# Performance work log

Hardware: AMD Instinct MI355X
Metric: run time of the kernel (lower is better)

Reference implementation:

```python
import jax, jax.numpy as jnp
import numpy as np

B, H_C, W_C = 4, 256, 256        # coarse mask logits
C, H_F, W_F = 128, 512, 512      # fine feature map
N_POINTS = 8192
HIDDEN = 256


def _grid_sample_bilinear(img, grid):
    """Bilinear grid_sample, align_corners=False, zeros padding.
    img: [C,H,W]; grid: [N,2] with (x,y) in [-1,1]. Returns [N,C]."""
    Ci, H, W = img.shape
    x = ((grid[:, 0] + 1.0) * W - 1.0) * 0.5
    y = ((grid[:, 1] + 1.0) * H - 1.0) * 0.5
    x0 = jnp.floor(x); y0 = jnp.floor(y)
    x1 = x0 + 1.0; y1 = y0 + 1.0
    wx1 = x - x0; wx0 = 1.0 - wx1
    wy1 = y - y0; wy0 = 1.0 - wy1

    def gather(xi, yi):
        valid = (xi >= 0) & (xi < W) & (yi >= 0) & (yi < H)
        xc = jnp.clip(xi, 0, W - 1).astype(jnp.int32)
        yc = jnp.clip(yi, 0, H - 1).astype(jnp.int32)
        v = img[:, yc, xc]                       # [C,N]
        return v * valid.astype(img.dtype)

    out = (gather(x0, y0) * (wx0 * wy0)
           + gather(x1, y0) * (wx1 * wy0)
           + gather(x0, y1) * (wx0 * wy1)
           + gather(x1, y1) * (wx1 * wy1))       # [C,N]
    return out.T                                  # [N,C]


def setup_inputs() -> dict:
    key = jax.random.key(0)
    k1, k2, k3, k4 = jax.random.split(key, 4)
    coarse_logits = jax.random.normal(k1, (B, 1, H_C, W_C), dtype=jnp.float32)
    fine_feat = jax.random.normal(k2, (B, C, H_F, W_F), dtype=jnp.float32)
    W1 = jax.random.normal(k3, (C + 1, HIDDEN), dtype=jnp.float32) * (1.0 / np.sqrt(C + 1))
    b1 = jnp.zeros((HIDDEN,), dtype=jnp.float32)
    W2 = jax.random.normal(k4, (HIDDEN, 1), dtype=jnp.float32) * (1.0 / np.sqrt(HIDDEN))
    b2 = jnp.zeros((1,), dtype=jnp.float32)
    return {"coarse_logits": coarse_logits, "fine_feat": fine_feat,
            "W1": W1, "b1": b1, "W2": W2, "b2": b2, "num_points": N_POINTS}


def reference(coarse_logits, fine_feat, W1, b1, W2, b2, num_points):
    b, _, h, w = coarse_logits.shape
    # uncertainty = -|logits|  (calculate_uncertainty)
    unc = -jnp.abs(coarse_logits[:, 0])                       # [B,h,w]
    _, idx = jax.lax.top_k(unc.reshape(b, -1), num_points)    # [B,N]
    # pixel-center normalized coords (sampling_points eval branch): (x,y) in [0,1]
    h_step, w_step = 1.0 / h, 1.0 / w
    px = w_step / 2.0 + (idx % w).astype(jnp.float32) * w_step
    py = h_step / 2.0 + (idx // w).astype(jnp.float32) * h_step
    grid = 2.0 * jnp.stack([px, py], axis=-1) - 1.0           # [B,N,2] in [-1,1]
    # point_sample: bilinear gather of fine features at sampled points
    fine_pts = jax.vmap(_grid_sample_bilinear)(fine_feat, grid)   # [B,N,C]
    # point_sample_by_idx: gather coarse logits at flat indices
    coarse_flat = coarse_logits.reshape(b, -1)                 # [B,h*w]
    coarse_pts = jnp.take_along_axis(coarse_flat, idx, axis=1)[..., None]  # [B,N,1]
    # point head MLP on concat(fine, coarse)
    feats = jnp.concatenate([fine_pts, coarse_pts], axis=-1)   # [B,N,C+1]
    hid = jax.nn.relu(jnp.einsum('bnf,fk->bnk', feats, W1) + b1)
    refined = jnp.einsum('bnk,ko->bno', hid, W2) + b2          # [B,N,1]
    # scatter refined logits back into the coarse map at sampled indices
    out_flat = coarse_flat.at[jnp.arange(b)[:, None], idx].set(refined[..., 0])
    return out_flat.reshape(b, 1, h, w)
```

## Files before the change

kernel.cpp:

```cpp
#include <hip/hip_runtime.h>
#include <stdint.h>

#define B_ 4
#define HC 256
#define WC 256
#define C_ 128
#define HF 512
#define WF 512
#define NPTS 8192
#define HIDDEN_ 256
#define NPIX (HC*WC)
#define PPB 16
#define FSTRIDE 132

__global__ void pr_copy_kernel(const float4* __restrict__ src, float4* __restrict__ dst, int n4) {
    int i = blockIdx.x * blockDim.x + threadIdx.x;
    if (i < n4) dst[i] = src[i];
}

__global__ __launch_bounds__(1024) void pr_select_kernel(const float* __restrict__ coarse,
                                                         int* __restrict__ sel) {
    int b = blockIdx.x;
    const float* cb = coarse + (size_t)b * NPIX;
    int tid = threadIdx.x;
    int lane = tid & 63, wid = tid >> 6;

    __shared__ unsigned hist[256];
    __shared__ unsigned s_prefix;
    __shared__ int s_remk;
    __shared__ unsigned wsum[16];
    __shared__ unsigned s_chosen, s_cless;
    __shared__ unsigned warp_eq[16], warp_take[16];
    __shared__ unsigned s_eqbase, s_outbase;

    if (tid == 0) { s_prefix = 0u; s_remk = NPTS; }

    for (int pass = 0; pass < 4; ++pass) {
        if (tid < 256) hist[tid] = 0u;
        __syncthreads();
        unsigned prefix = s_prefix;
        int remk = s_remk;
        int shift = 24 - 8 * pass;

        if (pass == 0) {
            for (int i = 4 * tid; i < NPIX; i += 4096) {
                float4 v = *(const float4*)(cb + i);
                unsigned bins[4];
                bins[0] = (__float_as_uint(v.x) & 0x7fffffffu) >> 24;
                bins[1] = (__float_as_uint(v.y) & 0x7fffffffu) >> 24;
                bins[2] = (__float_as_uint(v.z) & 0x7fffffffu) >> 24;
                bins[3] = (__float_as_uint(v.w) & 0x7fffffffu) >> 24;
#pragma unroll
                for (int e = 0; e < 4; ++e) {
                    unsigned bin = bins[e];
                    unsigned long long am = ~0ull;
                    while (am) {
                        int leader = __ffsll((unsigned long long)am) - 1;
                        unsigned lbin = __shfl(bin, leader, 64);
                        unsigned long long match = __ballot(bin == lbin);
                        if (lane == leader) atomicAdd(&hist[lbin], (unsigned)__popcll(match));
                        am &= ~match;
                    }
                }
            }
        } else {
            for (int i = 4 * tid; i < NPIX; i += 4096) {
                float4 v = *(const float4*)(cb + i);
                unsigned k0 = __float_as_uint(v.x) & 0x7fffffffu;
                unsigned k1 = __float_as_uint(v.y) & 0x7fffffffu;
                unsigned k2 = __float_as_uint(v.z) & 0x7fffffffu;
                unsigned k3 = __float_as_uint(v.w) & 0x7fffffffu;
                if ((k0 >> (shift + 8)) == prefix) atomicAdd(&hist[(k0 >> shift) & 0xffu], 1u);
                if ((k1 >> (shift + 8)) == prefix) atomicAdd(&hist[(k1 >> shift) & 0xffu], 1u);
                if ((k2 >> (shift + 8)) == prefix) atomicAdd(&hist[(k2 >> shift) & 0xffu], 1u);
                if ((k3 >> (shift + 8)) == prefix) atomicAdd(&hist[(k3 >> shift) & 0xffu], 1u);
            }
        }
        __syncthreads();

        unsigned h = 0, incl = 0;
        if (tid < 256) {
            h = hist[tid];
            incl = h;
#pragma unroll
            for (int d = 1; d < 64; d <<= 1) {
                unsigned y = __shfl_up(incl, d, 64);
                if (lane >= d) incl += y;
            }
            if (lane == 63) wsum[wid] = incl;
        }
        __syncthreads();
        if (tid < 256) {
            unsigned base = 0;
            for (int w = 0; w < wid; ++w) base += wsum[w];
            unsigned inc = base + incl;
            unsigned exc = inc - h;
            if ((unsigned)remk > exc && (unsigned)remk <= inc) { s_chosen = (unsigned)tid; s_cless = exc; }
        }
        __syncthreads();
        if (tid == 0) { s_prefix = (s_prefix << 8) | s_chosen; s_remk = remk - (int)s_cless; }
        __syncthreads();
    }

    unsigned T = s_prefix;
    unsigned need_eq = (unsigned)s_remk;
    if (tid == 0) { s_eqbase = 0u; s_outbase = 0u; }
    __syncthreads();

    unsigned long long ltmask = (1ull << lane) - 1ull;
    for (int base = 0; base < NPIX; base += 4096) {
        int i0 = base + 4 * tid;
        float4 v = *(const float4*)(cb + i0);
        unsigned k[4];
        k[0] = __float_as_uint(v.x) & 0x7fffffffu;
        k[1] = __float_as_uint(v.y) & 0x7fffffffu;
        k[2] = __float_as_uint(v.z) & 0x7fffffffu;
        k[3] = __float_as_uint(v.w) & 0x7fffffffu;
        bool lt[4], eq[4];
        unsigned long long me[4];
        unsigned weq = 0;
#pragma unroll
        for (int e = 0; e < 4; ++e) {
            lt[e] = k[e] < T;
            eq[e] = k[e] == T;
            me[e] = __ballot(eq[e]);
            weq += (unsigned)__popcll(me[e]);
        }
        if (lane == 0) warp_eq[wid] = weq;
        __syncthreads();

        unsigned eqwb = 0, eqtot = 0;
        for (int w = 0; w < 16; ++w) { unsigned hh = warp_eq[w]; if (w < wid) eqwb += hh; eqtot += hh; }
        unsigned lt_lanes_eq = 0;
#pragma unroll
        for (int e = 0; e < 4; ++e) lt_lanes_eq += (unsigned)__popcll(me[e] & ltmask);
        unsigned ebase = s_eqbase + eqwb + lt_lanes_eq;

        bool take[4];
        unsigned long long mt[4];
        unsigned self_eq = 0;
#pragma unroll
        for (int e = 0; e < 4; ++e) {
            unsigned eqrank = ebase + self_eq;
            take[e] = lt[e] || (eq[e] && eqrank < need_eq);
            self_eq += eq[e] ? 1u : 0u;
        }
        unsigned wtk = 0;
#pragma unroll
        for (int e = 0; e < 4; ++e) {
            mt[e] = __ballot(take[e]);
            wtk += (unsigned)__popcll(mt[e]);
        }
        if (lane == 0) warp_take[wid] = wtk;
        __syncthreads();

        unsigned twb = 0, ttot = 0;
        for (int w = 0; w < 16; ++w) { unsigned hh = warp_take[w]; if (w < wid) twb += hh; ttot += hh; }
        unsigned lt_lanes_tk = 0;
#pragma unroll
        for (int e = 0; e < 4; ++e) lt_lanes_tk += (unsigned)__popcll(mt[e] & ltmask);
        unsigned tbase = s_outbase + twb + lt_lanes_tk;
        unsigned self_tk = 0;
#pragma unroll
        for (int e = 0; e < 4; ++e) {
            if (take[e]) sel[b * NPTS + (int)(tbase + self_tk)] = i0 + e;
            self_tk += take[e] ? 1u : 0u;
        }
        __syncthreads();
        if (tid == 0) { s_eqbase += eqtot; s_outbase += ttot; }
    }
}

__global__ __launch_bounds__(256) void pr_mlp_kernel(
    const float* __restrict__ coarse, const float* __restrict__ fine,
    const float* __restrict__ W1, const float* __restrict__ b1,
    const float* __restrict__ W2, const float* __restrict__ b2,
    const int* __restrict__ sel, float* __restrict__ out) {

    __shared__ __align__(16) float feats[PPB * FSTRIDE];
    __shared__ int sidx[PPB];
    __shared__ float red[PPB][4];

    int tid = threadIdx.x;
    const int bpb = NPTS / PPB;
    int b = blockIdx.x / bpb;
    int pbase = (blockIdx.x % bpb) * PPB;

    if (tid < PPB) sidx[tid] = sel[b * NPTS + pbase + tid];
    __syncthreads();

    const float* fb = fine + (size_t)b * (C_ * HF * WF);
    int c = tid & 127;
    int ph = tid >> 7;

    float2 r0[PPB / 2], r1[PPB / 2];
#pragma unroll
    for (int k = 0; k < PPB / 2; ++k) {
        int p = 2 * k + ph;
        int id = sidx[p];
        int ix = id & (WC - 1), iy = id >> 8;
        const float* a = fb + (size_t)c * (HF * WF) + (size_t)(2 * iy) * WF + 2 * ix;
        r0[k] = *(const float2*)a;
        r1[k] = *(const float2*)(a + WF);
    }
#pragma unroll
    for (int k = 0; k < PPB / 2; ++k) {
        int p = 2 * k + ph;
        feats[p * FSTRIDE + c] = 0.25f * ((r0[k].x + r0[k].y) + (r1[k].x + r1[k].y));
    }
    if (tid < PPB) feats[tid * FSTRIDE + 128] = coarse[(size_t)b * NPIX + sidx[tid]];
    __syncthreads();

    int j = tid;
    float acc[PPB];
    float b1j = b1[j];
#pragma unroll
    for (int p = 0; p < PPB; ++p) acc[p] = b1j;

    const float4* fs4 = (const float4*)feats;
#pragma unroll 4
    for (int f4 = 0; f4 < 32; ++f4) {
        float w0 = W1[(4 * f4 + 0) * HIDDEN_ + j];
        float w1 = W1[(4 * f4 + 1) * HIDDEN_ + j];
        float w2 = W1[(4 * f4 + 2) * HIDDEN_ + j];
        float w3 = W1[(4 * f4 + 3) * HIDDEN_ + j];
#pragma unroll
        for (int p = 0; p < PPB; ++p) {
            float4 fv = fs4[p * (FSTRIDE / 4) + f4];
            acc[p] = fmaf(fv.x, w0, acc[p]);
            acc[p] = fmaf(fv.y, w1, acc[p]);
            acc[p] = fmaf(fv.z, w2, acc[p]);
            acc[p] = fmaf(fv.w, w3, acc[p]);
        }
    }
    {
        float w128 = W1[128 * HIDDEN_ + j];
#pragma unroll
        for (int p = 0; p < PPB; ++p) acc[p] = fmaf(feats[p * FSTRIDE + 128], w128, acc[p]);
    }

    float w2j = W2[j];
    int lane = tid & 63, wid = tid >> 6;
#pragma unroll
    for (int p = 0; p < PPB; ++p) {
        float v = fmaxf(acc[p], 0.0f) * w2j;
        v += __shfl_down(v, 32, 64);
        v += __shfl_down(v, 16, 64);
        v += __shfl_down(v, 8, 64);
        v += __shfl_down(v, 4, 64);
        v += __shfl_down(v, 2, 64);
        v += __shfl_down(v, 1, 64);
        if (lane == 0) red[p][wid] = v;
    }
    __syncthreads();
    if (tid < PPB) {
        float r = red[tid][0] + red[tid][1] + red[tid][2] + red[tid][3] + b2[0];
        out[(size_t)b * NPIX + sidx[tid]] = r;
    }
}

extern "C" void kernel_launch(void* const* d_in, const int* in_sizes, int n_in,
                              void* d_out, int out_size, void* d_ws, size_t ws_size,
                              hipStream_t stream) {
    const float* coarse = (const float*)d_in[0];
    const float* fine   = (const float*)d_in[1];
    const float* W1     = (const float*)d_in[2];
    const float* b1     = (const float*)d_in[3];
    const float* W2     = (const float*)d_in[4];
    const float* b2     = (const float*)d_in[5];
    float* out = (float*)d_out;
    int* sel = (int*)d_ws;

    int n4 = B_ * NPIX / 4;
    pr_copy_kernel<<<(n4 + 255) / 256, 256, 0, stream>>>((const float4*)coarse, (float4*)out, n4);
    pr_select_kernel<<<B_, 1024, 0, stream>>>(coarse, sel);
    pr_mlp_kernel<<<B_ * (NPTS / PPB), 256, 0, stream>>>(coarse, fine, W1, b1, W2, b2, sel, out);
}
```

Measured before the change: 797.0 us.

## Split gather from MLP, privatize select histograms, retile MLP per wave

The select kernel now keeps eight privatized shared-memory histograms (one per pair of waves) to reduce atomic contention, summing them before the prefix scan. The fused gather+MLP kernel is split in two. A gather kernel with 2 points per block writes 2x2-averaged fine features plus the coarse logit to a global workspace. An MLP kernel then has each wave handle 8 points with each lane owning 4 hidden units, using float4 W1 loads and no cross-wave reduction. This is meant to expose more parallelism for the scattered fine-feature loads and raise arithmetic intensity in the MLP. The cost is an extra global round trip for features and one more kernel launch.

```diff
diff --git a/kernel.cpp b/kernel.cpp
--- a/kernel.cpp
+++ b/kernel.cpp
@@ -10,8 +10,7 @@
 #define NPTS 8192
 #define HIDDEN_ 256
 #define NPIX (HC*WC)
-#define PPB 16
-#define FSTRIDE 132
+#define GSTRIDE 132
 
 __global__ void pr_copy_kernel(const float4* __restrict__ src, float4* __restrict__ dst, int n4) {
     int i = blockIdx.x * blockDim.x + threadIdx.x;
@@ -24,8 +23,9 @@
     const float* cb = coarse + (size_t)b * NPIX;
     int tid = threadIdx.x;
     int lane = tid & 63, wid = tid >> 6;
-
-    __shared__ unsigned hist[256];
+    int hc = wid >> 1;
+
+    __shared__ unsigned hist[8][256];
     __shared__ unsigned s_prefix;
     __shared__ int s_remk;
     __shared__ unsigned wsum[16];
@@ -36,7 +36,7 @@
     if (tid == 0) { s_prefix = 0u; s_remk = NPTS; }
 
     for (int pass = 0; pass < 4; ++pass) {
-        if (tid < 256) hist[tid] = 0u;
+        for (int i = tid; i < 2048; i += 1024) ((unsigned*)hist)[i] = 0u;
         __syncthreads();
         unsigned prefix = s_prefix;
         int remk = s_remk;
@@ -58,7 +58,7 @@
                         int leader = __ffsll((unsigned long long)am) - 1;
                         unsigned lbin = __shfl(bin, leader, 64);
                         unsigned long long match = __ballot(bin == lbin);
-                        if (lane == leader) atomicAdd(&hist[lbin], (unsigned)__popcll(match));
+                        if (lane == leader) atomicAdd(&hist[hc][lbin], (unsigned)__popcll(match));
                         am &= ~match;
                     }
                 }
@@ -70,17 +70,18 @@
                 unsigned k1 = __float_as_uint(v.y) & 0x7fffffffu;
                 unsigned k2 = __float_as_uint(v.z) & 0x7fffffffu;
                 unsigned k3 = __float_as_uint(v.w) & 0x7fffffffu;
-                if ((k0 >> (shift + 8)) == prefix) atomicAdd(&hist[(k0 >> shift) & 0xffu], 1u);
-                if ((k1 >> (shift + 8)) == prefix) atomicAdd(&hist[(k1 >> shift) & 0xffu], 1u);
-                if ((k2 >> (shift + 8)) == prefix) atomicAdd(&hist[(k2 >> shift) & 0xffu], 1u);
-                if ((k3 >> (shift + 8)) == prefix) atomicAdd(&hist[(k3 >> shift) & 0xffu], 1u);
+                if ((k0 >> (shift + 8)) == prefix) atomicAdd(&hist[hc][(k0 >> shift) & 0xffu], 1u);
+                if ((k1 >> (shift + 8)) == prefix) atomicAdd(&hist[hc][(k1 >> shift) & 0xffu], 1u);
+                if ((k2 >> (shift + 8)) == prefix) atomicAdd(&hist[hc][(k2 >> shift) & 0xffu], 1u);
+                if ((k3 >> (shift + 8)) == prefix) atomicAdd(&hist[hc][(k3 >> shift) & 0xffu], 1u);
             }
         }
         __syncthreads();
 
         unsigned h = 0, incl = 0;
         if (tid < 256) {
-            h = hist[tid];
+            h = hist[0][tid] + hist[1][tid] + hist[2][tid] + hist[3][tid]
+              + hist[4][tid] + hist[5][tid] + hist[6][tid] + hist[7][tid];
             incl = h;
 #pragma unroll
             for (int d = 1; d < 64; d <<= 1) {
@@ -171,91 +172,105 @@
     }
 }
 
+__global__ __launch_bounds__(256) void pr_gather_kernel(
+    const float* __restrict__ coarse, const float* __restrict__ fine,
+    const int* __restrict__ sel, float* __restrict__ feats) {
+    int tid = threadIdx.x;
+    int b = blockIdx.x >> 12;
+    int pbase = (blockIdx.x & 4095) * 2;
+    __shared__ int sidx[2];
+    if (tid < 2) sidx[tid] = sel[b * NPTS + pbase + tid];
+    __syncthreads();
+    int c = tid & 127, ph = tid >> 7;
+    int id = sidx[ph];
+    int ix = id & (WC - 1), iy = id >> 8;
+    const float* a = fine + (size_t)(b * C_ + c) * (HF * WF) + (size_t)(2 * iy) * WF + 2 * ix;
+    float2 r0 = *(const float2*)a;
+    float2 r1 = *(const float2*)(a + WF);
+    size_t o = (size_t)(b * NPTS + pbase + ph) * GSTRIDE;
+    feats[o + c] = 0.25f * ((r0.x + r0.y) + (r1.x + r1.y));
+    if (c == 0) feats[o + 128] = coarse[(size_t)b * NPIX + id];
+}
+
 __global__ __launch_bounds__(256) void pr_mlp_kernel(
-    const float* __restrict__ coarse, const float* __restrict__ fine,
-    const float* __restrict__ W1, const float* __restrict__ b1,
-    const float* __restrict__ W2, const float* __restrict__ b2,
-    const int* __restrict__ sel, float* __restrict__ out) {
-
-    __shared__ __align__(16) float feats[PPB * FSTRIDE];
-    __shared__ int sidx[PPB];
-    __shared__ float red[PPB][4];
-
+    const float* __restrict__ feats, const float* __restrict__ W1,
+    const float* __restrict__ b1, const float* __restrict__ W2,
+    const float* __restrict__ b2, const int* __restrict__ sel,
+    float* __restrict__ out) {
+    __shared__ int sidx[32];
     int tid = threadIdx.x;
-    const int bpb = NPTS / PPB;
-    int b = blockIdx.x / bpb;
-    int pbase = (blockIdx.x % bpb) * PPB;
-
-    if (tid < PPB) sidx[tid] = sel[b * NPTS + pbase + tid];
+    int b = blockIdx.x >> 8;
+    int pbase = (blockIdx.x & 255) * 32;
+    if (tid < 32) sidx[tid] = sel[b * NPTS + pbase + tid];
     __syncthreads();
 
-    const float* fb = fine + (size_t)b * (C_ * HF * WF);
-    int c = tid & 127;
-    int ph = tid >> 7;
-
-    float2 r0[PPB / 2], r1[PPB / 2];
-#pragma unroll
-    for (int k = 0; k < PPB / 2; ++k) {
-        int p = 2 * k + ph;
-        int id = sidx[p];
-        int ix = id & (WC - 1), iy = id >> 8;
-        const float* a = fb + (size_t)c * (HF * WF) + (size_t)(2 * iy) * WF + 2 * ix;
-        r0[k] = *(const float2*)a;
-        r1[k] = *(const float2*)(a + WF);
-    }
-#pragma unroll
-    for (int k = 0; k < PPB / 2; ++k) {
-        int p = 2 * k + ph;
-        feats[p * FSTRIDE + c] = 0.25f * ((r0[k].x + r0[k].y) + (r1[k].x + r1[k].y));
-    }
-    if (tid < PPB) feats[tid * FSTRIDE + 128] = coarse[(size_t)b * NPIX + sidx[tid]];
-    __syncthreads();
-
-    int j = tid;
-    float acc[PPB];
-    float b1j = b1[j];
-#pragma unroll
-    for (int p = 0; p < PPB; ++p) acc[p] = b1j;
-
-    const float4* fs4 = (const float4*)feats;
-#pragma unroll 4
+    int lane = tid & 63, wv = tid >> 6;
+    float4 b14 = *(const float4*)&b1[4 * lane];
+    float acc[8][4];
+#pragma unroll
+    for (int i = 0; i < 8; ++i) {
+        acc[i][0] = b14.x; acc[i][1] = b14.y; acc[i][2] = b14.z; acc[i][3] = b14.w;
+    }
+
+    const float* frow = feats + (size_t)(b * NPTS + pbase + wv * 8) * GSTRIDE;
+    const float4* f4p = (const float4*)frow;
+
     for (int f4 = 0; f4 < 32; ++f4) {
-        float w0 = W1[(4 * f4 + 0) * HIDDEN_ + j];
-        float w1 = W1[(4 * f4 + 1) * HIDDEN_ + j];
-        float w2 = W1[(4 * f4 + 2) * HIDDEN_ + j];
-        float w3 = W1[(4 * f4 + 3) * HIDDEN_ + j];
-#pragma unroll
-        for (int p = 0; p < PPB; ++p) {
-            float4 fv = fs4[p * (FSTRIDE / 4) + f4];
-            acc[p] = fmaf(fv.x, w0, acc[p]);
-            acc[p] = fmaf(fv.y, w1, acc[p]);
-            acc[p] = fmaf(fv.z, w2, acc[p]);
-            acc[p] = fmaf(fv.w, w3, acc[p]);
+        float4 w0 = *(const float4*)&W1[(4 * f4 + 0) * HIDDEN_ + 4 * lane];
+        float4 w1v = *(const float4*)&W1[(4 * f4 + 1) * HIDDEN_ + 4 * lane];
+        float4 w2v = *(const float4*)&W1[(4 * f4 + 2) * HIDDEN_ + 4 * lane];
+        float4 w3v = *(const float4*)&W1[(4 * f4 + 3) * HIDDEN_ + 4 * lane];
+#pragma unroll
+        for (int i = 0; i < 8; ++i) {
+            float4 fv = f4p[i * 33 + f4];
+            acc[i][0] = fmaf(fv.x, w0.x, acc[i][0]);
+            acc[i][1] = fmaf(fv.x, w0.y, acc[i][1]);
+            acc[i][2] = fmaf(fv.x, w0.z, acc[i][2]);
+            acc[i][3] = fmaf(fv.x, w0.w, acc[i][3]);
+            acc[i][0] = fmaf(fv.y, w1v.x, acc[i][0]);
+            acc[i][1] = fmaf(fv.y, w1v.y, acc[i][1]);
+            acc[i][2] = fmaf(fv.y, w1v.z, acc[i][2]);
+            acc[i][3] = fmaf(fv.y, w1v.w, acc[i][3]);
+            acc[i][0] = fmaf(fv.z, w2v.x, acc[i][0]);
+            acc[i][1] = fmaf(fv.z, w2v.y, acc[i][1]);
+            acc[i][2] = fmaf(fv.z, w2v.z, acc[i][2]);
+            acc[i][3] = fmaf(fv.z, w2v.w, acc[i][3]);
+            acc[i][0] = fmaf(fv.w, w3v.x, acc[i][0]);
+            acc[i][1] = fmaf(fv.w, w3v.y, acc[i][1]);
+            acc[i][2] = fmaf(fv.w, w3v.z, acc[i][2]);
+            acc[i][3] = fmaf(fv.w, w3v.w, acc[i][3]);
         }
     }
     {
-        float w128 = W1[128 * HIDDEN_ + j];
-#pragma unroll
-        for (int p = 0; p < PPB; ++p) acc[p] = fmaf(feats[p * FSTRIDE + 128], w128, acc[p]);
-    }
-
-    float w2j = W2[j];
-    int lane = tid & 63, wid = tid >> 6;
-#pragma unroll
-    for (int p = 0; p < PPB; ++p) {
-        float v = fmaxf(acc[p], 0.0f) * w2j;
+        float4 wl = *(const float4*)&W1[128 * HIDDEN_ + 4 * lane];
+#pragma unroll
+        for (int i = 0; i < 8; ++i) {
+            float fc = frow[i * GSTRIDE + 128];
+            acc[i][0] = fmaf(fc, wl.x, acc[i][0]);
+            acc[i][1] = fmaf(fc, wl.y, acc[i][1]);
+            acc[i][2] = fmaf(fc, wl.z, acc[i][2]);
+            acc[i][3] = fmaf(fc, wl.w, acc[i][3]);
+        }
+    }
+
+    float4 w2f = *(const float4*)&W2[4 * lane];
+    float bb = b2[0];
+#pragma unroll
+    for (int i = 0; i < 8; ++i) {
+        float v = fmaxf(acc[i][0], 0.0f) * w2f.x
+                + fmaxf(acc[i][1], 0.0f) * w2f.y
+                + fmaxf(acc[i][2], 0.0f) * w2f.z
+                + fmaxf(acc[i][3], 0.0f) * w2f.w;
         v += __shfl_down(v, 32, 64);
         v += __shfl_down(v, 16, 64);
         v += __shfl_down(v, 8, 64);
         v += __shfl_down(v, 4, 64);
         v += __shfl_down(v, 2, 64);
         v += __shfl_down(v, 1, 64);
-        if (lane == 0) red[p][wid] = v;
-    }
-    __syncthreads();
-    if (tid < PPB) {
-        float r = red[tid][0] + red[tid][1] + red[tid][2] + red[tid][3] + b2[0];
-        out[(size_t)b * NPIX + sidx[tid]] = r;
+        if (lane == 0) {
+            int id = sidx[wv * 8 + i];
+            out[(size_t)b * NPIX + id] = v + bb;
+        }
     }
 }
 
@@ -270,9 +285,11 @@
     const float* b2     = (const float*)d_in[5];
     float* out = (float*)d_out;
     int* sel = (int*)d_ws;
+    float* feats = (float*)((char*)d_ws + (1 << 20));
 
     int n4 = B_ * NPIX / 4;
     pr_copy_kernel<<<(n4 + 255) / 256, 256, 0, stream>>>((const float4*)coarse, (float4*)out, n4);
     pr_select_kernel<<<B_, 1024, 0, stream>>>(coarse, sel);
-    pr_mlp_kernel<<<B_ * (NPTS / PPB), 256, 0, stream>>>(coarse, fine, W1, b1, W2, b2, sel, out);
-}
+    pr_gather_kernel<<<B_ * (NPTS / 2), 256, 0, stream>>>(coarse, fine, sel, feats);
+    pr_mlp_kernel<<<B_ * (NPTS / 32), 256, 0, stream>>>(feats, W1, b1, W2, b2, sel, out);
+}
```

Result: slower. 824.6 us (+3.5%).
